# Optimization experiments

Measured on AMD Instinct MI355X. Metric: run time of the kernel, lower is better.

## Reference

```python
import jax, jax.numpy as jnp
import numpy as np

N = 50000   # nodes
E = 800000  # edges
IN, HID, HEADS, OUT = 128, 32, 4, 64
NEG_SLOPE = 0.2


def _gatv2_layer(x, src, dst, Wl, bl, Wr, br, att, bias, res_W, concat):
    """One PyG-style GATv2Conv layer (eval mode, no dropout).
    x: [N, F_in]; att: [H, C]. Returns [N, H*C] if concat else [N, C]."""
    H, C = att.shape
    xl = (x @ Wl + bl).reshape(N, H, C)   # source transform
    xr = (x @ Wr + br).reshape(N, H, C)   # target transform
    e = jax.nn.leaky_relu(xl[src] + xr[dst], NEG_SLOPE)        # [E, H, C]
    logit = jnp.einsum('ehc,hc->eh', e, att)                   # [E, H]
    # segment softmax over incoming edges per destination node
    m = jax.ops.segment_max(logit, dst, num_segments=N)        # [N, H]
    p = jnp.exp(logit - m[dst])
    denom = jax.ops.segment_sum(p, dst, num_segments=N)
    alpha = p / (denom[dst] + 1e-16)                           # [E, H]
    out = jax.ops.segment_sum(xl[src] * alpha[:, :, None], dst, num_segments=N)  # [N, H, C]
    out = out.reshape(N, H * C) if concat else out.mean(axis=1)
    if res_W is not None:
        out = out + x @ res_W
    return out + bias


def _glorot(key, shape):
    fan_in = shape[0] if len(shape) > 1 else shape[-1]
    return jax.random.normal(key, shape, dtype=jnp.float32) / np.sqrt(fan_in)


def setup_inputs() -> dict:
    key = jax.random.key(0)
    ks = iter(jax.random.split(key, 32))
    x = jax.random.normal(next(ks), (N, IN), dtype=jnp.float32)
    edge_index = jax.random.randint(next(ks), (2, E), 0, N, dtype=jnp.int64)
    d = {"x": x, "edge_index": edge_index}
    HC = HEADS * HID  # 128
    # layer 0: IN -> HEADS*HID, concat, residual
    d["Wl0"] = _glorot(next(ks), (IN, HC)); d["bl0"] = jnp.zeros((HC,), jnp.float32)
    d["Wr0"] = _glorot(next(ks), (IN, HC)); d["br0"] = jnp.zeros((HC,), jnp.float32)
    d["att0"] = _glorot(next(ks), (HEADS, HID)); d["b0"] = jnp.zeros((HC,), jnp.float32)
    d["res0"] = _glorot(next(ks), (IN, HC))
    # layer 1: HC -> HEADS*HID, concat, residual
    d["Wl1"] = _glorot(next(ks), (HC, HC)); d["bl1"] = jnp.zeros((HC,), jnp.float32)
    d["Wr1"] = _glorot(next(ks), (HC, HC)); d["br1"] = jnp.zeros((HC,), jnp.float32)
    d["att1"] = _glorot(next(ks), (HEADS, HID)); d["b1"] = jnp.zeros((HC,), jnp.float32)
    d["res1"] = _glorot(next(ks), (HC, HC))
    # layer 2: HC -> OUT, heads=1, concat=False, no residual
    d["Wl2"] = _glorot(next(ks), (HC, OUT)); d["bl2"] = jnp.zeros((OUT,), jnp.float32)
    d["Wr2"] = _glorot(next(ks), (HC, OUT)); d["br2"] = jnp.zeros((OUT,), jnp.float32)
    d["att2"] = _glorot(next(ks), (1, OUT)); d["b2"] = jnp.zeros((OUT,), jnp.float32)
    return d


def reference(x, edge_index,
              Wl0, bl0, Wr0, br0, att0, b0, res0,
              Wl1, bl1, Wr1, br1, att1, b1, res1,
              Wl2, bl2, Wr2, br2, att2, b2):
    src, dst = edge_index[0], edge_index[1]
    h = _gatv2_layer(x, src, dst, Wl0, bl0, Wr0, br0, att0, b0, res0, True)
    h = jax.nn.elu(h)
    h = _gatv2_layer(h, src, dst, Wl1, bl1, Wr1, br1, att1, b1, res1, True)
    h = jax.nn.elu(h)
    return _gatv2_layer(h, src, dst, Wl2, bl2, Wr2, br2, att2, b2, None, False)
```

## Files before the change

### kernel.cpp

```cpp
#include <hip/hip_runtime.h>
#include <math.h>

#define NN 50000
#define EE 800000
#define NBK 196
#define EPB 4096

typedef short v8s __attribute__((ext_vector_type(8)));
typedef float v4f __attribute__((ext_vector_type(4)));

__device__ __forceinline__ ushort f2bf(float f) {
    uint u = __float_as_uint(f);
    uint r = (u + 0x7fffu + ((u >> 16) & 1u)) >> 16;
    return (ushort)r;
}
__device__ __forceinline__ float bf2f(ushort h) {
    return __uint_as_float(((uint)h) << 16);
}
__device__ __forceinline__ float lrelu(float x) {
    return fmaf(0.4f, fabsf(x), 0.6f * x);
}

template <int CTRL>
__device__ __forceinline__ float dppadd(float x) {
    int y = __builtin_amdgcn_update_dpp(0, __float_as_int(x), CTRL, 0xf, 0xf, true);
    return x + __int_as_float(y);
}
__device__ __forceinline__ float sum8(float x) {
    x = dppadd<0xB1>(x);
    x = dppadd<0x4E>(x);
    x = dppadd<0x141>(x);
    return x;
}
__device__ __forceinline__ float sum16(float x) {
    x = sum8(x);
    x = dppadd<0x140>(x);
    return x;
}
__device__ __forceinline__ float expclamp(float t) {
    return __expf(fminf(fmaxf(t, -60.f), 80.f));
}

__global__ __launch_bounds__(256) void k_bktcnt(const int* __restrict__ edst,
                                                int* __restrict__ bcnt) {
    __shared__ int h[NBK];
    int t = threadIdx.x;
    if (t < NBK) h[t] = 0;
    __syncthreads();
    int eb = blockIdx.x * EPB;
    #pragma unroll
    for (int k = 0; k < EPB / 256; ++k) {
        int e = eb + k * 256 + t;
        if (e < EE) atomicAdd(&h[edst[e] >> 8], 1);
    }
    __syncthreads();
    if (t < NBK && h[t]) atomicAdd(&bcnt[t], h[t]);
}

__global__ __launch_bounds__(256) void k_bscan(const int* __restrict__ bcnt,
                                               int* __restrict__ bbase,
                                               int* __restrict__ bcur) {
    __shared__ int sm[256];
    int t = threadIdx.x;
    int v = (t < NBK) ? bcnt[t] : 0;
    sm[t] = v;
    __syncthreads();
    for (int o = 1; o < 256; o <<= 1) {
        int a = (t >= o) ? sm[t - o] : 0;
        __syncthreads();
        sm[t] += a;
        __syncthreads();
    }
    if (t < NBK) { int ex = sm[t] - v; bbase[t] = ex; bcur[t] = ex; }
}

__global__ __launch_bounds__(256) void k_bktplace(const int* __restrict__ esrc,
                                                  const int* __restrict__ edst,
                                                  int* __restrict__ bcur,
                                                  uint* __restrict__ ebuf) {
    __shared__ int h[NBK];
    __shared__ int base[NBK];
    int t = threadIdx.x;
    if (t < NBK) h[t] = 0;
    __syncthreads();
    int eb = blockIdx.x * EPB;
    int pk[EPB / 256];
    #pragma unroll
    for (int k = 0; k < EPB / 256; ++k) {
        int e = eb + k * 256 + t;
        pk[k] = -1;
        if (e < EE) {
            int b = edst[e] >> 8;
            int r = atomicAdd(&h[b], 1);
            pk[k] = (b << 16) | r;
        }
    }
    __syncthreads();
    if (t < NBK && h[t]) base[t] = atomicAdd(&bcur[t], h[t]);
    __syncthreads();
    #pragma unroll
    for (int k = 0; k < EPB / 256; ++k) {
        int e = eb + k * 256 + t;
        if (e < EE) {
            int b = pk[k] >> 16;
            int r = pk[k] & 0xFFFF;
            uint dl = (uint)(edst[e] & 255);
            ebuf[base[b] + r] = (dl << 16) | (uint)esrc[e];
        }
    }
}

__global__ __launch_bounds__(256) void k_bktfin(const uint* __restrict__ ebuf,
                                                const int* __restrict__ bbase,
                                                const int* __restrict__ bcnt,
                                                int* __restrict__ rowptr,
                                                int* __restrict__ csrc) {
    __shared__ int deg[256];
    __shared__ int sm[256];
    __shared__ int cur[256];
    const int b = blockIdx.x;
    const int t = threadIdx.x;
    const int eb = bbase[b];
    const int ec = bcnt[b];
    deg[t] = 0;
    __syncthreads();
    for (int k = t; k < ec; k += 256)
        atomicAdd(&deg[ebuf[eb + k] >> 16], 1);
    __syncthreads();
    int v = deg[t];
    sm[t] = v;
    __syncthreads();
    for (int o = 1; o < 256; o <<= 1) {
        int a = (t >= o) ? sm[t - o] : 0;
        __syncthreads();
        sm[t] += a;
        __syncthreads();
    }
    int node = b * 256 + t;
    if (node < NN) rowptr[node + 1] = eb + sm[t];
    if (node == 0) rowptr[0] = 0;
    cur[t] = sm[t] - v;
    __syncthreads();
    for (int k = t; k < ec; k += 256) {
        uint u = ebuf[eb + k];
        int nl = (int)(u >> 16);
        int r = atomicAdd(&cur[nl], 1);
        csrc[eb + r] = (int)(u & 0xFFFFu);
    }
}

struct WPack {
    const float* W[8];
    ushort* Th[8];
    ushort* Tl[8];
    int fout[8];
};

__global__ __launch_bounds__(256) void k_conv_w(WPack p) {
    int wi = blockIdx.y;
    int fout = p.fout[wi];
    int total = 128 * fout;
    int i = blockIdx.x * 256 + threadIdx.x;
    if (i >= total) return;
    int k = i / fout;
    int n = i - k * fout;
    float f = p.W[wi][i];
    ushort h = f2bf(f);
    float lo = f - bf2f(h);
    int t = n >> 4, m = n & 15, c = k >> 5, quad = (k >> 3) & 3, j = k & 7;
    int flat = ((((t * 4 + c) * 4 + quad) * 16 + m) << 3) + j;
    p.Th[wi][flat] = h;
    p.Tl[wi][flat] = f2bf(lo);
}

template <int FOUT, int NMAT, bool CVT>
__global__ __launch_bounds__(256) void k_gemm_fused(
    const float* __restrict__ Xf,
    const ushort* __restrict__ Xh, const ushort* __restrict__ Xl,
    const ushort* __restrict__ T0h, const ushort* __restrict__ T0l, const float* __restrict__ B0,
    const ushort* __restrict__ T1h, const ushort* __restrict__ T1l, const float* __restrict__ B1,
    const ushort* __restrict__ T2h, const ushort* __restrict__ T2l,
    ushort* __restrict__ O0b, float* __restrict__ O1, float* __restrict__ O2)
{
    const int lane = threadIdx.x & 63;
    const int wid  = threadIdx.x >> 6;
    const int m    = lane & 15;
    const int quad = lane >> 4;
    const int row0 = blockIdx.x * 64 + wid * 16;

    v8s ah[4], al[4];
    {
        int arow = row0 + m;
        if (arow > NN - 1) arow = NN - 1;
        #pragma unroll
        for (int c = 0; c < 4; ++c) {
            size_t off = (size_t)arow * 128 + c * 32 + quad * 8;
            if constexpr (CVT) {
                float4 f0 = *(const float4*)(Xf + off);
                float4 f1 = *(const float4*)(Xf + off + 4);
                const float fe[8] = {f0.x, f0.y, f0.z, f0.w, f1.x, f1.y, f1.z, f1.w};
                #pragma unroll
                for (int e = 0; e < 8; ++e) {
                    ushort h = f2bf(fe[e]);
                    float lo = fe[e] - bf2f(h);
                    ah[c][e] = (short)h;
                    al[c][e] = (short)(__float_as_uint(lo) >> 16);
                }
            } else {
                ah[c] = *(const v8s*)(Xh + off);
                al[c] = *(const v8s*)(Xl + off);
            }
        }
    }

    #pragma unroll
    for (int t = 0; t < FOUT / 16; ++t) {
        v4f a0 = {0.f, 0.f, 0.f, 0.f};
        v4f a1 = {0.f, 0.f, 0.f, 0.f};
        v4f a2 = {0.f, 0.f, 0.f, 0.f};
        #pragma unroll
        for (int c = 0; c < 4; ++c) {
            const int boff = t * 2048 + (c * 4 + quad) * 128 + m * 8;
            v8s b0h = *(const v8s*)(T0h + boff);
            v8s b0l = *(const v8s*)(T0l + boff);
            v8s b1h = *(const v8s*)(T1h + boff);
            v8s b1l = *(const v8s*)(T1l + boff);
            a0 = __builtin_amdgcn_mfma_f32_16x16x32_bf16(al[c], b0h, a0, 0, 0, 0);
            a1 = __builtin_amdgcn_mfma_f32_16x16x32_bf16(al[c], b1h, a1, 0, 0, 0);
            a0 = __builtin_amdgcn_mfma_f32_16x16x32_bf16(ah[c], b0l, a0, 0, 0, 0);
            a1 = __builtin_amdgcn_mfma_f32_16x16x32_bf16(ah[c], b1l, a1, 0, 0, 0);
            a0 = __builtin_amdgcn_mfma_f32_16x16x32_bf16(ah[c], b0h, a0, 0, 0, 0);
            a1 = __builtin_amdgcn_mfma_f32_16x16x32_bf16(ah[c], b1h, a1, 0, 0, 0);
            if constexpr (NMAT == 3) {
                v8s b2h = *(const v8s*)(T2h + boff);
                v8s b2l = *(const v8s*)(T2l + boff);
                a2 = __builtin_amdgcn_mfma_f32_16x16x32_bf16(al[c], b2h, a2, 0, 0, 0);
                a2 = __builtin_amdgcn_mfma_f32_16x16x32_bf16(ah[c], b2l, a2, 0, 0, 0);
                a2 = __builtin_amdgcn_mfma_f32_16x16x32_bf16(ah[c], b2h, a2, 0, 0, 0);
            }
        }
        const int col = t * 16 + m;
        const float bad0 = B0[col];
        const float bad1 = B1[col];
        #pragma unroll
        for (int j = 0; j < 4; ++j) {
            int r = row0 + quad * 4 + j;
            if (r < NN) {
                O0b[(size_t)r * FOUT + col] = f2bf(a0[j] + bad0);
                O1[(size_t)r * FOUT + col] = a1[j] + bad1;
                if constexpr (NMAT == 3) O2[(size_t)r * FOUT + col] = a2[j];
            }
        }
    }
}

__global__ __launch_bounds__(256) void k_agg01(const ushort* __restrict__ XLb,
                                               const float4* __restrict__ XR4,
                                               const float4* __restrict__ RES4,
                                               const float* __restrict__ att,
                                               const float* __restrict__ bias,
                                               const int* __restrict__ rowptr,
                                               const int* __restrict__ csrc,
                                               ushort* __restrict__ Hh,
                                               ushort* __restrict__ Hl) {
    const int lane = threadIdx.x & 63;
    const int wid = threadIdx.x >> 6;
    const int n = blockIdx.x * 4 + wid;
    if (n >= NN) return;
    const int beg = rowptr[n];
    const int end = rowptr[n + 1];
    const int half = lane >> 5;
    const uint j = lane & 31;

    const float4 xr = XR4[(uint)n * 32u + j];
    const float4 at = ((const float4*)att)[j];
    float4 s = {0.f, 0.f, 0.f, 0.f};
    float d = 0.f;

    int i = beg;
    for (; i + 4 <= end; i += 4) {
        uint sa = (uint)csrc[i + half];
        uint sb = (uint)csrc[i + 2 + half];
        ushort4 ua = *(const ushort4*)(XLb + sa * 128u + 4u * j);
        ushort4 ub = *(const ushort4*)(XLb + sb * 128u + 4u * j);
        {
            float4 va = {bf2f(ua.x), bf2f(ua.y), bf2f(ua.z), bf2f(ua.w)};
            float t0 = lrelu(va.x + xr.x) * at.x;
            t0 = fmaf(lrelu(va.y + xr.y), at.y, t0);
            t0 = fmaf(lrelu(va.z + xr.z), at.z, t0);
            t0 = fmaf(lrelu(va.w + xr.w), at.w, t0);
            float p = expclamp(sum8(t0));
            d += p;
            s.x = fmaf(p, va.x, s.x); s.y = fmaf(p, va.y, s.y);
            s.z = fmaf(p, va.z, s.z); s.w = fmaf(p, va.w, s.w);
        }
        {
            float4 vb = {bf2f(ub.x), bf2f(ub.y), bf2f(ub.z), bf2f(ub.w)};
            float t0 = lrelu(vb.x + xr.x) * at.x;
            t0 = fmaf(lrelu(vb.y + xr.y), at.y, t0);
            t0 = fmaf(lrelu(vb.z + xr.z), at.z, t0);
            t0 = fmaf(lrelu(vb.w + xr.w), at.w, t0);
            float p = expclamp(sum8(t0));
            d += p;
            s.x = fmaf(p, vb.x, s.x); s.y = fmaf(p, vb.y, s.y);
            s.z = fmaf(p, vb.z, s.z); s.w = fmaf(p, vb.w, s.w);
        }
    }
    for (; i < end; i += 2) {
        int ia = i + half;
        if (ia > end - 1) ia = end - 1;
        uint sa = (uint)csrc[ia];
        ushort4 ua = *(const ushort4*)(XLb + sa * 128u + 4u * j);
        float4 va = {bf2f(ua.x), bf2f(ua.y), bf2f(ua.z), bf2f(ua.w)};
        float t0 = lrelu(va.x + xr.x) * at.x;
        t0 = fmaf(lrelu(va.y + xr.y), at.y, t0);
        t0 = fmaf(lrelu(va.z + xr.z), at.z, t0);
        t0 = fmaf(lrelu(va.w + xr.w), at.w, t0);
        float p = expclamp(sum8(t0));
        if (half && (i + 1 >= end)) p = 0.f;
        d += p;
        s.x = fmaf(p, va.x, s.x); s.y = fmaf(p, va.y, s.y);
        s.z = fmaf(p, va.z, s.z); s.w = fmaf(p, va.w, s.w);
    }

    d   += __shfl_xor(d, 32);
    s.x += __shfl_xor(s.x, 32);
    s.y += __shfl_xor(s.y, 32);
    s.z += __shfl_xor(s.z, 32);
    s.w += __shfl_xor(s.w, 32);

    if (half == 0) {
        float inv = (d > 0.f) ? 1.f / d : 0.f;
        float4 rv = RES4[(uint)n * 32u + j];
        float4 bv = ((const float4*)bias)[j];
        float o0 = fmaf(s.x, inv, rv.x + bv.x);
        float o1 = fmaf(s.y, inv, rv.y + bv.y);
        float o2 = fmaf(s.z, inv, rv.z + bv.z);
        float o3 = fmaf(s.w, inv, rv.w + bv.w);
        o0 = o0 > 0.f ? o0 : __expf(o0) - 1.f;
        o1 = o1 > 0.f ? o1 : __expf(o1) - 1.f;
        o2 = o2 > 0.f ? o2 : __expf(o2) - 1.f;
        o3 = o3 > 0.f ? o3 : __expf(o3) - 1.f;
        ushort4 h, l;
        h.x = f2bf(o0); l.x = f2bf(o0 - bf2f(h.x));
        h.y = f2bf(o1); l.y = f2bf(o1 - bf2f(h.y));
        h.z = f2bf(o2); l.z = f2bf(o2 - bf2f(h.z));
        h.w = f2bf(o3); l.w = f2bf(o3 - bf2f(h.w));
        *(ushort4*)(Hh + (uint)n * 128u + 4u * j) = h;
        *(ushort4*)(Hl + (uint)n * 128u + 4u * j) = l;
    }
}

__global__ __launch_bounds__(256) void k_agg2(const ushort* __restrict__ XLb,
                                              const float4* __restrict__ XR4,
                                              const float* __restrict__ att,
                                              const float* __restrict__ bias,
                                              const int* __restrict__ rowptr,
                                              const int* __restrict__ csrc,
                                              float* __restrict__ OUT) {
    const int lane = threadIdx.x & 63;
    const int wid = threadIdx.x >> 6;
    const int n = blockIdx.x * 4 + wid;
    if (n >= NN) return;
    const int beg = rowptr[n];
    const int end = rowptr[n + 1];
    const int q = lane >> 4;
    const uint jj = lane & 15;

    const float4 xr = XR4[(uint)n * 16u + jj];
    const float4 at = ((const float4*)att)[jj];
    float4 s = {0.f, 0.f, 0.f, 0.f};
    float d = 0.f;
    const int e1 = end - 1;

    for (int i = beg; i < end; i += 8) {
        int i0 = i + q;
        int i1 = i + 4 + q;
        uint s0 = (uint)csrc[min(i0, e1)];
        uint s1 = (uint)csrc[min(i1, e1)];
        ushort4 u0 = *(const ushort4*)(XLb + s0 * 64u + 4u * jj);
        ushort4 u1 = *(const ushort4*)(XLb + s1 * 64u + 4u * jj);
        #pragma unroll
        for (int u = 0; u < 2; ++u) {
            ushort4 uv = (u == 0) ? u0 : u1;
            int ii = (u == 0) ? i0 : i1;
            float4 v = {bf2f(uv.x), bf2f(uv.y), bf2f(uv.z), bf2f(uv.w)};
            float t0 = lrelu(v.x + xr.x) * at.x;
            t0 = fmaf(lrelu(v.y + xr.y), at.y, t0);
            t0 = fmaf(lrelu(v.z + xr.z), at.z, t0);
            t0 = fmaf(lrelu(v.w + xr.w), at.w, t0);
            float p = expclamp(sum16(t0));
            if (ii >= end) p = 0.f;
            d += p;
            s.x = fmaf(p, v.x, s.x); s.y = fmaf(p, v.y, s.y);
            s.z = fmaf(p, v.z, s.z); s.w = fmaf(p, v.w, s.w);
        }
    }

    d   += __shfl_xor(d, 16);   d   += __shfl_xor(d, 32);
    s.x += __shfl_xor(s.x, 16); s.x += __shfl_xor(s.x, 32);
    s.y += __shfl_xor(s.y, 16); s.y += __shfl_xor(s.y, 32);
    s.z += __shfl_xor(s.z, 16); s.z += __shfl_xor(s.z, 32);
    s.w += __shfl_xor(s.w, 16); s.w += __shfl_xor(s.w, 32);

    if (lane < 16) {
        float inv = (d > 0.f) ? 1.f / d : 0.f;
        float4 bv = ((const float4*)bias)[jj];
        float4 o;
        o.x = fmaf(s.x, inv, bv.x);
        o.y = fmaf(s.y, inv, bv.y);
        o.z = fmaf(s.z, inv, bv.z);
        o.w = fmaf(s.w, inv, bv.w);
        *(float4*)(OUT + (uint)n * 64u + 4u * jj) = o;
    }
}

extern "C" void kernel_launch(void* const* d_in, const int* in_sizes, int n_in,
                              void* d_out, int out_size, void* d_ws, size_t ws_size,
                              hipStream_t stream) {
    const float* x    = (const float*)d_in[0];
    const int*   ei   = (const int*)d_in[1];
    const int*   esrc = ei;
    const int*   edst = ei + EE;

    const float* Wl0 = (const float*)d_in[2];
    const float* bl0 = (const float*)d_in[3];
    const float* Wr0 = (const float*)d_in[4];
    const float* br0 = (const float*)d_in[5];
    const float* at0 = (const float*)d_in[6];
    const float* b0  = (const float*)d_in[7];
    const float* rs0 = (const float*)d_in[8];
    const float* Wl1 = (const float*)d_in[9];
    const float* bl1 = (const float*)d_in[10];
    const float* Wr1 = (const float*)d_in[11];
    const float* br1 = (const float*)d_in[12];
    const float* at1 = (const float*)d_in[13];
    const float* b1  = (const float*)d_in[14];
    const float* rs1 = (const float*)d_in[15];
    const float* Wl2 = (const float*)d_in[16];
    const float* bl2 = (const float*)d_in[17];
    const float* Wr2 = (const float*)d_in[18];
    const float* br2 = (const float*)d_in[19];
    const float* at2 = (const float*)d_in[20];
    const float* b2  = (const float*)d_in[21];

    float* out = (float*)d_out;

    ushort* XLb = (ushort*)d_ws;
    float* XR  = (float*)(XLb + (size_t)NN * 128);
    float* RES = XR + (size_t)NN * 128;
    ushort* Xh = (ushort*)(RES + (size_t)NN * 128);
    ushort* Xl_ = Xh + (size_t)NN * 128;
    ushort* Wth = Xl_ + (size_t)NN * 128;
    const int wsz[8] = {16384, 16384, 16384, 16384, 16384, 16384, 8192, 8192};
    ushort* th[8]; ushort* tl[8];
    {
        ushort* p = Wth;
        for (int i = 0; i < 8; ++i) { th[i] = p; p += wsz[i]; }
        for (int i = 0; i < 8; ++i) { tl[i] = p; p += wsz[i]; }
    }
    int* bcnt   = (int*)(Wth + 2 * (6 * 16384 + 2 * 8192));
    int* bbase  = bcnt + 256;
    int* bcur   = bbase + 256;
    int* rowptr = bcur + 256;
    int* csrc   = rowptr + (NN + 1);
    uint* ebuf  = (uint*)(csrc + EE);

    hipMemsetAsync(bcnt, 0, 256 * sizeof(int), stream);
    const int ebk = (EE + EPB - 1) / EPB;
    k_bktcnt<<<ebk, 256, 0, stream>>>(edst, bcnt);
    k_bscan<<<1, 256, 0, stream>>>(bcnt, bbase, bcur);
    k_bktplace<<<ebk, 256, 0, stream>>>(esrc, edst, bcur, ebuf);
    k_bktfin<<<NBK, 256, 0, stream>>>(ebuf, bbase, bcnt, rowptr, csrc);

    WPack wp;
    const float* Ws[8] = {Wl0, Wr0, rs0, Wl1, Wr1, rs1, Wl2, Wr2};
    const int fouts[8] = {128, 128, 128, 128, 128, 128, 64, 64};
    for (int i = 0; i < 8; ++i) { wp.W[i] = Ws[i]; wp.Th[i] = th[i]; wp.Tl[i] = tl[i]; wp.fout[i] = fouts[i]; }
    k_conv_w<<<dim3(64, 8), 256, 0, stream>>>(wp);

    const int gemm_gx = (NN + 63) / 64;
    const int agg_grid = (NN + 3) / 4;

    k_gemm_fused<128, 3, true><<<gemm_gx, 256, 0, stream>>>(x, nullptr, nullptr,
        th[0], tl[0], bl0, th[1], tl[1], br0, th[2], tl[2], XLb, XR, RES);
    k_agg01<<<agg_grid, 256, 0, stream>>>(XLb, (const float4*)XR, (const float4*)RES,
        at0, b0, rowptr, csrc, Xh, Xl_);

    k_gemm_fused<128, 3, false><<<gemm_gx, 256, 0, stream>>>(nullptr, Xh, Xl_,
        th[3], tl[3], bl1, th[4], tl[4], br1, th[5], tl[5], XLb, XR, RES);
    k_agg01<<<agg_grid, 256, 0, stream>>>(XLb, (const float4*)XR, (const float4*)RES,
        at1, b1, rowptr, csrc, Xh, Xl_);

    k_gemm_fused<64, 2, false><<<gemm_gx, 256, 0, stream>>>(nullptr, Xh, Xl_,
        th[6], tl[6], bl2, th[7], tl[7], br2, nullptr, nullptr, XLb, XR, nullptr);
    k_agg2<<<agg_grid, 256, 0, stream>>>(XLb, (const float4*)XR, at2, b2, rowptr, csrc, out);
}
```

Before: 355.2 us.

## Split leaky-ReLU into linear and abs terms, precompute per-node attention dot products

Rewrites leaky_relu(x) as 0.6x + 0.4|x|, so the linear part of the attention logit becomes per-node dot products att·xl and att·xr. These are computed in the GEMM epilogue and stored, the source-side value padded into each XL row and the target-side value in a separate DR array. The edge loop then only evaluates the abs term plus two scalars, and the main edge loop is unrolled from 4 to 8 edges. This saves per-edge ALU work but grows XL rows (136/68 elements) and adds a scalar load per edge. The linear-part dot product now uses fp32 GEMM outputs rather than the bf16-rounded xl, which slightly changes numerics.

```diff
diff --git a/kernel.cpp b/kernel.cpp
--- a/kernel.cpp
+++ b/kernel.cpp
@@ -180,8 +180,14 @@
     const ushort* __restrict__ T0h, const ushort* __restrict__ T0l, const float* __restrict__ B0,
     const ushort* __restrict__ T1h, const ushort* __restrict__ T1l, const float* __restrict__ B1,
     const ushort* __restrict__ T2h, const ushort* __restrict__ T2l,
+    const float* __restrict__ ATT, float* __restrict__ DR,
     ushort* __restrict__ O0b, float* __restrict__ O1, float* __restrict__ O2)
 {
+    constexpr int NH  = (FOUT == 128) ? 4 : 1;
+    constexpr int RS  = FOUT + ((FOUT == 128) ? 8 : 4);
+    constexpr int NT  = FOUT / 16;
+    constexpr int TPH = NT / NH;
+
     const int lane = threadIdx.x & 63;
     const int wid  = threadIdx.x >> 6;
     const int m    = lane & 15;
@@ -213,8 +219,11 @@
         }
     }
 
+    float dp0[4] = {0.f, 0.f, 0.f, 0.f};
+    float dp1[4] = {0.f, 0.f, 0.f, 0.f};
+
     #pragma unroll
-    for (int t = 0; t < FOUT / 16; ++t) {
+    for (int t = 0; t < NT; ++t) {
         v4f a0 = {0.f, 0.f, 0.f, 0.f};
         v4f a1 = {0.f, 0.f, 0.f, 0.f};
         v4f a2 = {0.f, 0.f, 0.f, 0.f};
@@ -242,13 +251,33 @@
         const int col = t * 16 + m;
         const float bad0 = B0[col];
         const float bad1 = B1[col];
+        const float attc = ATT[col];
         #pragma unroll
         for (int j = 0; j < 4; ++j) {
+            float o0v = a0[j] + bad0;
+            float o1v = a1[j] + bad1;
+            dp0[j] = fmaf(attc, o0v, dp0[j]);
+            dp1[j] = fmaf(attc, o1v, dp1[j]);
             int r = row0 + quad * 4 + j;
             if (r < NN) {
-                O0b[(size_t)r * FOUT + col] = f2bf(a0[j] + bad0);
-                O1[(size_t)r * FOUT + col] = a1[j] + bad1;
+                O0b[(size_t)r * RS + col] = f2bf(o0v);
+                O1[(size_t)r * FOUT + col] = o1v;
                 if constexpr (NMAT == 3) O2[(size_t)r * FOUT + col] = a2[j];
+            }
+        }
+        if ((t % TPH) == TPH - 1) {
+            const int h = t / TPH;
+            #pragma unroll
+            for (int j = 0; j < 4; ++j) {
+                float s0 = sum16(dp0[j]);
+                float s1 = sum16(dp1[j]);
+                int r = row0 + quad * 4 + j;
+                if (m == 0 && r < NN) {
+                    *(float*)(O0b + (size_t)r * RS + FOUT + 2 * h) = 0.6f * s0;
+                    DR[(size_t)r * NH + h] = 0.6f * s1;
+                }
+                dp0[j] = 0.f;
+                dp1[j] = 0.f;
             }
         }
     }
@@ -259,6 +288,7 @@
                                                const float4* __restrict__ RES4,
                                                const float* __restrict__ att,
                                                const float* __restrict__ bias,
+                                               const float* __restrict__ DR,
                                                const int* __restrict__ rowptr,
                                                const int* __restrict__ csrc,
                                                ushort* __restrict__ Hh,
@@ -271,57 +301,68 @@
     const int end = rowptr[n + 1];
     const int half = lane >> 5;
     const uint j = lane & 31;
+    const int head = (int)(j >> 3);
 
     const float4 xr = XR4[(uint)n * 32u + j];
-    const float4 at = ((const float4*)att)[j];
+    float4 at = ((const float4*)att)[j];
+    at.x *= 0.4f; at.y *= 0.4f; at.z *= 0.4f; at.w *= 0.4f;
+    const float dRn = DR[(uint)n * 4u + (uint)head];
     float4 s = {0.f, 0.f, 0.f, 0.f};
     float d = 0.f;
 
+#define EDGE01(U, DL)  {                                              \
+    float4 v = {bf2f((U).x), bf2f((U).y), bf2f((U).z), bf2f((U).w)};  \
+    float t0 =      at.x * fabsf(v.x + xr.x);                         \
+    t0 = fmaf(at.y, fabsf(v.y + xr.y), t0);                           \
+    t0 = fmaf(at.z, fabsf(v.z + xr.z), t0);                           \
+    t0 = fmaf(at.w, fabsf(v.w + xr.w), t0);                           \
+    float p = expclamp(sum8(t0) + (DL) + dRn);                        \
+    d += p;                                                            \
+    s.x = fmaf(p, v.x, s.x); s.y = fmaf(p, v.y, s.y);                 \
+    s.z = fmaf(p, v.z, s.z); s.w = fmaf(p, v.w, s.w); }
+
     int i = beg;
-    for (; i + 4 <= end; i += 4) {
+    for (; i + 8 <= end; i += 8) {
         uint sa = (uint)csrc[i + half];
         uint sb = (uint)csrc[i + 2 + half];
-        ushort4 ua = *(const ushort4*)(XLb + sa * 128u + 4u * j);
-        ushort4 ub = *(const ushort4*)(XLb + sb * 128u + 4u * j);
-        {
-            float4 va = {bf2f(ua.x), bf2f(ua.y), bf2f(ua.z), bf2f(ua.w)};
-            float t0 = lrelu(va.x + xr.x) * at.x;
-            t0 = fmaf(lrelu(va.y + xr.y), at.y, t0);
-            t0 = fmaf(lrelu(va.z + xr.z), at.z, t0);
-            t0 = fmaf(lrelu(va.w + xr.w), at.w, t0);
-            float p = expclamp(sum8(t0));
-            d += p;
-            s.x = fmaf(p, va.x, s.x); s.y = fmaf(p, va.y, s.y);
-            s.z = fmaf(p, va.z, s.z); s.w = fmaf(p, va.w, s.w);
-        }
-        {
-            float4 vb = {bf2f(ub.x), bf2f(ub.y), bf2f(ub.z), bf2f(ub.w)};
-            float t0 = lrelu(vb.x + xr.x) * at.x;
-            t0 = fmaf(lrelu(vb.y + xr.y), at.y, t0);
-            t0 = fmaf(lrelu(vb.z + xr.z), at.z, t0);
-            t0 = fmaf(lrelu(vb.w + xr.w), at.w, t0);
-            float p = expclamp(sum8(t0));
-            d += p;
-            s.x = fmaf(p, vb.x, s.x); s.y = fmaf(p, vb.y, s.y);
-            s.z = fmaf(p, vb.z, s.z); s.w = fmaf(p, vb.w, s.w);
-        }
+        uint sc = (uint)csrc[i + 4 + half];
+        uint sd = (uint)csrc[i + 6 + half];
+        const ushort* pa = XLb + (size_t)sa * 136u;
+        const ushort* pb = XLb + (size_t)sb * 136u;
+        const ushort* pc = XLb + (size_t)sc * 136u;
+        const ushort* pd = XLb + (size_t)sd * 136u;
+        ushort4 ua = *(const ushort4*)(pa + 4u * j);
+        float  da_ = *(const float*)(pa + 128 + 2 * head);
+        ushort4 ub = *(const ushort4*)(pb + 4u * j);
+        float  db_ = *(const float*)(pb + 128 + 2 * head);
+        ushort4 uc = *(const ushort4*)(pc + 4u * j);
+        float  dc_ = *(const float*)(pc + 128 + 2 * head);
+        ushort4 ud = *(const ushort4*)(pd + 4u * j);
+        float  dd_ = *(const float*)(pd + 128 + 2 * head);
+        EDGE01(ua, da_)
+        EDGE01(ub, db_)
+        EDGE01(uc, dc_)
+        EDGE01(ud, dd_)
     }
     for (; i < end; i += 2) {
         int ia = i + half;
         if (ia > end - 1) ia = end - 1;
         uint sa = (uint)csrc[ia];
-        ushort4 ua = *(const ushort4*)(XLb + sa * 128u + 4u * j);
-        float4 va = {bf2f(ua.x), bf2f(ua.y), bf2f(ua.z), bf2f(ua.w)};
-        float t0 = lrelu(va.x + xr.x) * at.x;
-        t0 = fmaf(lrelu(va.y + xr.y), at.y, t0);
-        t0 = fmaf(lrelu(va.z + xr.z), at.z, t0);
-        t0 = fmaf(lrelu(va.w + xr.w), at.w, t0);
-        float p = expclamp(sum8(t0));
+        const ushort* pa = XLb + (size_t)sa * 136u;
+        ushort4 ua = *(const ushort4*)(pa + 4u * j);
+        float  da_ = *(const float*)(pa + 128 + 2 * head);
+        float4 v = {bf2f(ua.x), bf2f(ua.y), bf2f(ua.z), bf2f(ua.w)};
+        float t0 =      at.x * fabsf(v.x + xr.x);
+        t0 = fmaf(at.y, fabsf(v.y + xr.y), t0);
+        t0 = fmaf(at.z, fabsf(v.z + xr.z), t0);
+        t0 = fmaf(at.w, fabsf(v.w + xr.w), t0);
+        float p = expclamp(sum8(t0) + da_ + dRn);
         if (half && (i + 1 >= end)) p = 0.f;
         d += p;
-        s.x = fmaf(p, va.x, s.x); s.y = fmaf(p, va.y, s.y);
-        s.z = fmaf(p, va.z, s.z); s.w = fmaf(p, va.w, s.w);
-    }
+        s.x = fmaf(p, v.x, s.x); s.y = fmaf(p, v.y, s.y);
+        s.z = fmaf(p, v.z, s.z); s.w = fmaf(p, v.w, s.w);
+    }
+#undef EDGE01
 
     d   += __shfl_xor(d, 32);
     s.x += __shfl_xor(s.x, 32);
@@ -355,6 +396,7 @@
                                               const float4* __restrict__ XR4,
                                               const float* __restrict__ att,
                                               const float* __restrict__ bias,
+                                              const float* __restrict__ DR,
                                               const int* __restrict__ rowptr,
                                               const int* __restrict__ csrc,
                                               float* __restrict__ OUT) {
@@ -368,7 +410,9 @@
     const uint jj = lane & 15;
 
     const float4 xr = XR4[(uint)n * 16u + jj];
-    const float4 at = ((const float4*)att)[jj];
+    float4 at = ((const float4*)att)[jj];
+    at.x *= 0.4f; at.y *= 0.4f; at.z *= 0.4f; at.w *= 0.4f;
+    const float dRn = DR[n];
     float4 s = {0.f, 0.f, 0.f, 0.f};
     float d = 0.f;
     const int e1 = end - 1;
@@ -378,18 +422,23 @@
         int i1 = i + 4 + q;
         uint s0 = (uint)csrc[min(i0, e1)];
         uint s1 = (uint)csrc[min(i1, e1)];
-        ushort4 u0 = *(const ushort4*)(XLb + s0 * 64u + 4u * jj);
-        ushort4 u1 = *(const ushort4*)(XLb + s1 * 64u + 4u * jj);
+        const ushort* p0 = XLb + (size_t)s0 * 68u;
+        const ushort* p1 = XLb + (size_t)s1 * 68u;
+        ushort4 u0 = *(const ushort4*)(p0 + 4u * jj);
+        float  dl0 = *(const float*)(p0 + 64);
+        ushort4 u1 = *(const ushort4*)(p1 + 4u * jj);
+        float  dl1 = *(const float*)(p1 + 64);
         #pragma unroll
         for (int u = 0; u < 2; ++u) {
             ushort4 uv = (u == 0) ? u0 : u1;
+            float  dlv = (u == 0) ? dl0 : dl1;
             int ii = (u == 0) ? i0 : i1;
             float4 v = {bf2f(uv.x), bf2f(uv.y), bf2f(uv.z), bf2f(uv.w)};
-            float t0 = lrelu(v.x + xr.x) * at.x;
-            t0 = fmaf(lrelu(v.y + xr.y), at.y, t0);
-            t0 = fmaf(lrelu(v.z + xr.z), at.z, t0);
-            t0 = fmaf(lrelu(v.w + xr.w), at.w, t0);
-            float p = expclamp(sum16(t0));
+            float t0 =      at.x * fabsf(v.x + xr.x);
+            t0 = fmaf(at.y, fabsf(v.y + xr.y), t0);
+            t0 = fmaf(at.z, fabsf(v.z + xr.z), t0);
+            t0 = fmaf(at.w, fabsf(v.w + xr.w), t0);
+            float p = expclamp(sum16(t0) + dlv + dRn);
             if (ii >= end) p = 0.f;
             d += p;
             s.x = fmaf(p, v.x, s.x); s.y = fmaf(p, v.y, s.y);
@@ -447,11 +496,12 @@
     float* out = (float*)d_out;
 
     ushort* XLb = (ushort*)d_ws;
-    float* XR  = (float*)(XLb + (size_t)NN * 128);
+    float* XR  = (float*)(XLb + (size_t)NN * 136);
     float* RES = XR + (size_t)NN * 128;
     ushort* Xh = (ushort*)(RES + (size_t)NN * 128);
     ushort* Xl_ = Xh + (size_t)NN * 128;
-    ushort* Wth = Xl_ + (size_t)NN * 128;
+    float* DRarr = (float*)(Xl_ + (size_t)NN * 128);
+    ushort* Wth = (ushort*)(DRarr + (size_t)NN * 4);
     const int wsz[8] = {16384, 16384, 16384, 16384, 16384, 16384, 8192, 8192};
     ushort* th[8]; ushort* tl[8];
     {
@@ -483,16 +533,16 @@
     const int agg_grid = (NN + 3) / 4;
 
     k_gemm_fused<128, 3, true><<<gemm_gx, 256, 0, stream>>>(x, nullptr, nullptr,
-        th[0], tl[0], bl0, th[1], tl[1], br0, th[2], tl[2], XLb, XR, RES);
+        th[0], tl[0], bl0, th[1], tl[1], br0, th[2], tl[2], at0, DRarr, XLb, XR, RES);
     k_agg01<<<agg_grid, 256, 0, stream>>>(XLb, (const float4*)XR, (const float4*)RES,
-        at0, b0, rowptr, csrc, Xh, Xl_);
+        at0, b0, DRarr, rowptr, csrc, Xh, Xl_);
 
     k_gemm_fused<128, 3, false><<<gemm_gx, 256, 0, stream>>>(nullptr, Xh, Xl_,
-        th[3], tl[3], bl1, th[4], tl[4], br1, th[5], tl[5], XLb, XR, RES);
+        th[3], tl[3], bl1, th[4], tl[4], br1, th[5], tl[5], at1, DRarr, XLb, XR, RES);
     k_agg01<<<agg_grid, 256, 0, stream>>>(XLb, (const float4*)XR, (const float4*)RES,
-        at1, b1, rowptr, csrc, Xh, Xl_);
+        at1, b1, DRarr, rowptr, csrc, Xh, Xl_);
 
     k_gemm_fused<64, 2, false><<<gemm_gx, 256, 0, stream>>>(nullptr, Xh, Xl_,
-        th[6], tl[6], bl2, th[7], tl[7], br2, nullptr, nullptr, XLb, XR, nullptr);
-    k_agg2<<<agg_grid, 256, 0, stream>>>(XLb, (const float4*)XR, at2, b2, rowptr, csrc, out);
-}
+        th[6], tl[6], bl2, th[7], tl[7], br2, nullptr, nullptr, at2, DRarr, XLb, XR, nullptr);
+    k_agg2<<<agg_grid, 256, 0, stream>>>(XLb, (const float4*)XR, at2, b2, DRarr, rowptr, csrc, out);
+}
```

Measured after the change: 365.5 us. +2.9%, slower.
